# Kernel tuning notes

Hardware: AMD Instinct MI355X
Metric: run time of the kernel (lower is better)

The kernel has to match this reference:

```python
import jax, jax.numpy as jnp
import numpy as np

B, C, H, W = 2, 512, 64, 64
NH = 8
EPS = 1e-5


def setup_inputs() -> dict:
    key = jax.random.key(0)
    ks = jax.random.split(key, 4)
    s_in = 1.0 / np.sqrt(C)
    x = jax.random.normal(ks[0], (B, C, H, W), dtype=jnp.float32)
    qkv_w = jax.random.normal(ks[1], (3 * C, C), dtype=jnp.float32) * s_in
    qkv_b = jnp.zeros((3 * C,), dtype=jnp.float32)
    out_w = jax.random.normal(ks[2], (C, C), dtype=jnp.float32) * s_in
    out_b = jnp.zeros((C,), dtype=jnp.float32)
    ln_g = jnp.ones((C,), dtype=jnp.float32)
    ln_b = jnp.zeros((C,), dtype=jnp.float32)
    return {"x": x, "qkv_w": qkv_w, "qkv_b": qkv_b, "out_w": out_w,
            "out_b": out_b, "ln_g": ln_g, "ln_b": ln_b, "num_heads": NH}


def reference(x, qkv_w, qkv_b, out_w, out_b, ln_g, ln_b, num_heads):
    b, c, h, w = x.shape
    n = h * w
    hd = c // num_heads
    scale = hd ** -0.5

    # flatten spatial: [B, N, C]
    tokens = x.reshape(b, c, n).transpose(0, 2, 1)

    # fused QKV projection
    qkv = tokens @ qkv_w.T + qkv_b            # [B, N, 3C]
    q, k, v = jnp.split(qkv, 3, axis=-1)

    def heads(t):  # [B, N, C] -> [B, H, N, D]
        return t.reshape(b, n, num_heads, hd).transpose(0, 2, 1, 3)

    q, k, v = heads(q), heads(k), heads(v)

    # naive full attention (materializes [B, H, N, N] as in the original)
    scores = jnp.einsum('bhqd,bhkd->bhqk', q, k) * scale
    attn = jax.nn.softmax(scores, axis=-1)
    out = jnp.einsum('bhqk,bhkd->bhqd', attn, v)  # [B, H, N, D]

    out = out.transpose(0, 2, 1, 3).reshape(b, n, c)
    attended = out @ out_w.T + out_b          # [B, N, C]

    # residual + LayerNorm over channels
    res = attended + tokens
    mean = jnp.mean(res, axis=-1, keepdims=True)
    var = jnp.var(res, axis=-1, keepdims=True)
    y = (res - mean) * jax.lax.rsqrt(var + EPS) * ln_g + ln_b

    return y.transpose(0, 2, 1).reshape(b, c, h, w)
```

## Files before the change

### kernel.cpp

```cpp
#include <hip/hip_runtime.h>

#define BATCH 2
#define CH    512
#define NTOK  4096
#define NH    8
#define HD    64
#define MTOT  (BATCH*NTOK)

typedef __attribute__((ext_vector_type(8))) __bf16 bf16x8;
typedef __attribute__((ext_vector_type(4))) float  f32x4;
typedef __attribute__((ext_vector_type(4))) unsigned short u16x4;

static __device__ __forceinline__ f32x4 mfma16(bf16x8 a, bf16x8 b, f32x4 c) {
  return __builtin_amdgcn_mfma_f32_16x16x32_bf16(a, b, c, 0, 0, 0);
}

static __device__ __forceinline__ unsigned short f2bf(float f) {
  unsigned int u = __float_as_uint(f);
  u += 0x7fffu + ((u >> 16) & 1u);
  return (unsigned short)(u >> 16);
}

static __device__ __forceinline__ void gload_lds16(const unsigned short* g, unsigned short* l) {
  __builtin_amdgcn_global_load_lds((const __attribute__((address_space(1))) void*)g,
                                   (__attribute__((address_space(3))) void*)l, 16, 0, 0);
}

#define QSC 0.18033688011112042f

__global__ __launch_bounds__(256) void k_transpose(const float* __restrict__ x,
                                                   unsigned short* __restrict__ tokB) {
  __shared__ float tile[32][33];
  int b  = blockIdx.z;
  int n0 = blockIdx.x * 32;
  int c0 = blockIdx.y * 32;
  int tx = threadIdx.x & 31, ty = threadIdx.x >> 5;
#pragma unroll
  for (int i = 0; i < 4; i++) {
    int c = c0 + ty + 8 * i;
    tile[ty + 8 * i][tx] = x[((size_t)b * CH + c) * NTOK + n0 + tx];
  }
  __syncthreads();
#pragma unroll
  for (int i = 0; i < 4; i++) {
    int n = n0 + ty + 8 * i;
    int c = c0 + tx;
    tokB[((size_t)b * NTOK + n) * CH + c] = f2bf(tile[tx][ty + 8 * i]);
  }
}

__global__ __launch_bounds__(256) void k_castw(const float* __restrict__ w1,
                                               const float* __restrict__ w2,
                                               unsigned short* __restrict__ o1,
                                               unsigned short* __restrict__ o2) {
  int i = blockIdx.x * 256 + threadIdx.x;
  if (i < 3 * CH * CH) o1[i] = f2bf(w1[i]);
  else o2[i - 3 * CH * CH] = f2bf(w2[i - 3 * CH * CH]);
}

#define BK 64

static __device__ __forceinline__ void stage_g(const unsigned short* __restrict__ src,
                                               size_t row0, int k0,
                                               unsigned short* __restrict__ lds,
                                               int wid, int lane) {
  int sub = lane >> 3;
  int ch  = (lane & 7) ^ sub;
#pragma unroll
  for (int i = 0; i < 4; i++) {
    int rbase = 32 * wid + 8 * i;
    gload_lds16(&src[(row0 + rbase + sub) * 512 + k0 + ch * 8], &lds[rbase * BK]);
  }
}

static __device__ __forceinline__ bf16x8 frag_ld(const unsigned short* __restrict__ lds,
                                                 int row, int ks, int lane) {
  int ch = ((ks << 2) + (lane >> 4)) ^ (row & 7);
  return *reinterpret_cast<const bf16x8*>(&lds[row * BK + ch * 8]);
}

__global__ __launch_bounds__(256) void k_gemm_qkv(const unsigned short* __restrict__ A,
                                                  const unsigned short* __restrict__ W,
                                                  const float* __restrict__ bias,
                                                  unsigned short* __restrict__ qb,
                                                  unsigned short* __restrict__ kb,
                                                  unsigned short* __restrict__ vt) {
  __shared__ unsigned short lsA[128 * BK];
  __shared__ unsigned short lsB[128 * BK];
  int bm0 = blockIdx.x * 128;
  int bn0 = blockIdx.y * 128;
  int tid = threadIdx.x, lane = tid & 63, wid = tid >> 6;
  int wm = wid >> 1, wn = wid & 1;

  f32x4 acc[4][4];
  f32x4 zz = {0.f, 0.f, 0.f, 0.f};
#pragma unroll
  for (int i = 0; i < 4; i++)
#pragma unroll
    for (int j = 0; j < 4; j++) acc[i][j] = zz;

  for (int k0 = 0; k0 < 512; k0 += BK) {
    stage_g(A, (size_t)bm0, k0, lsA, wid, lane);
    stage_g(W, (size_t)bn0, k0, lsB, wid, lane);
    __syncthreads();
#pragma unroll
    for (int ks = 0; ks < 2; ks++) {
      bf16x8 af[4], bfr[4];
#pragma unroll
      for (int t = 0; t < 4; t++) {
        af[t]  = frag_ld(lsA, wm * 64 + t * 16 + (lane & 15), ks, lane);
        bfr[t] = frag_ld(lsB, wn * 64 + t * 16 + (lane & 15), ks, lane);
      }
#pragma unroll
      for (int mt = 0; mt < 4; mt++)
#pragma unroll
        for (int nt = 0; nt < 4; nt++) acc[mt][nt] = mfma16(af[mt], bfr[nt], acc[mt][nt]);
    }
    __syncthreads();
  }
#pragma unroll
  for (int nt = 0; nt < 4; nt++) {
    int j = bn0 + wn * 64 + nt * 16 + (lane & 15);
    float bj = bias[j];
    int which = j >> 9;
    int cp = j & 511;
    int h = cp >> 6, d = cp & 63;
    if (which == 2) {
#pragma unroll
      for (int mt = 0; mt < 4; mt++) {
        int m = bm0 + wm * 64 + mt * 16 + 4 * (lane >> 4);
        int b = m >> 12, n = m & 4095;
        u16x4 pk;
#pragma unroll
        for (int r = 0; r < 4; r++) pk[r] = f2bf(acc[mt][nt][r] + bj);
        *reinterpret_cast<u16x4*>(&vt[((size_t)((b * NH + h) * HD + d)) * NTOK + n]) = pk;
      }
    } else {
      unsigned short* dst = (which == 0) ? qb : kb;
      float sc = (which == 0) ? QSC : 1.0f;
#pragma unroll
      for (int mt = 0; mt < 4; mt++) {
#pragma unroll
        for (int r = 0; r < 4; r++) {
          int m = bm0 + wm * 64 + mt * 16 + 4 * (lane >> 4) + r;
          int b = m >> 12, n = m & 4095;
          dst[(((size_t)(b * NH + h) * NTOK + n) << 6) + d] = f2bf((acc[mt][nt][r] + bj) * sc);
        }
      }
    }
  }
}

#define KVB 64
#define NT  (NTOK / KVB)

static __device__ __forceinline__ void stage_kv(const unsigned short* __restrict__ Kp,
                                                const unsigned short* __restrict__ Vp,
                                                unsigned short* __restrict__ lk,
                                                unsigned short* __restrict__ lv,
                                                int kv0, int wid, int lane) {
  int sub = lane >> 3;
  int c7  = lane & 7;
#pragma unroll
  for (int i = 0; i < 2; i++) {
    int rbase = 16 * wid + 8 * i;
    int row = rbase + sub;
    int fk = (sub & 3) | (i << 2);
    gload_lds16(&Kp[((size_t)(kv0 + row) << 6) + ((c7 ^ fk) << 3)], &lk[rbase << 6]);
    gload_lds16(&Vp[(size_t)row * NTOK + kv0 + ((c7 ^ sub) << 3)], &lv[rbase << 6]);
  }
}

static __device__ __forceinline__ void attn_tile(const unsigned short* __restrict__ lk,
                                                 const unsigned short* __restrict__ lv,
                                                 const bf16x8 qf[2][2],
                                                 f32x4* oacc0, f32x4* oacc1,
                                                 f32x4& lacc0, f32x4& lacc1,
                                                 bf16x8 onesf, int g, int lr) {
  f32x4 zz = {0.f, 0.f, 0.f, 0.f};
  int l7 = lr & 7;
  int tbase = 8 * (lr >> 2) + (lr & 3);
  int kc0 = ((g ^ l7) << 3);
  int kc1 = (((4 + g) ^ l7) << 3);
  bf16x8 kf[4][2];
#pragma unroll
  for (int ct = 0; ct < 4; ct++) {
    int t = tbase + 4 * (ct >> 1) + 32 * (ct & 1);
    kf[ct][0] = *reinterpret_cast<const bf16x8*>(&lk[(t << 6) + kc0]);
    kf[ct][1] = *reinterpret_cast<const bf16x8*>(&lk[(t << 6) + kc1]);
  }
  f32x4 s0[4], s1[4];
#pragma unroll
  for (int ct = 0; ct < 4; ct++) {
    s0[ct] = zz; s1[ct] = zz;
#pragma unroll
    for (int ks = 0; ks < 2; ks++) {
      s0[ct] = mfma16(kf[ct][ks], qf[0][ks], s0[ct]);
      s1[ct] = mfma16(kf[ct][ks], qf[1][ks], s1[ct]);
    }
  }
  bf16x8 vf[4][2];
#pragma unroll
  for (int dt = 0; dt < 4; dt++) {
    vf[dt][0] = *reinterpret_cast<const bf16x8*>(&lv[((dt * 16 + lr) << 6) + kc0]);
    vf[dt][1] = *reinterpret_cast<const bf16x8*>(&lv[((dt * 16 + lr) << 6) + kc1]);
  }
#pragma unroll
  for (int ct = 0; ct < 4; ct++) {
#pragma unroll
    for (int r = 0; r < 4; r++) {
      s0[ct][r] = __builtin_exp2f(s0[ct][r]);
      s1[ct][r] = __builtin_exp2f(s1[ct][r]);
    }
  }
  unsigned int w0[4][2], w1[4][2];
#pragma unroll
  for (int ct = 0; ct < 4; ct++) {
    asm("v_cvt_pk_bf16_f32 %0, %1, %2" : "=v"(w0[ct][0]) : "v"(s0[ct][0]), "v"(s0[ct][1]));
    asm("v_cvt_pk_bf16_f32 %0, %1, %2" : "=v"(w0[ct][1]) : "v"(s0[ct][2]), "v"(s0[ct][3]));
    asm("v_cvt_pk_bf16_f32 %0, %1, %2" : "=v"(w1[ct][0]) : "v"(s1[ct][0]), "v"(s1[ct][1]));
    asm("v_cvt_pk_bf16_f32 %0, %1, %2" : "=v"(w1[ct][1]) : "v"(s1[ct][2]), "v"(s1[ct][3]));
  }
  union U { unsigned int w[4]; bf16x8 v; };
  U a0, a1, b0, b1;
  a0.w[0] = w0[0][0]; a0.w[1] = w0[0][1]; a0.w[2] = w0[2][0]; a0.w[3] = w0[2][1];
  a1.w[0] = w0[1][0]; a1.w[1] = w0[1][1]; a1.w[2] = w0[3][0]; a1.w[3] = w0[3][1];
  b0.w[0] = w1[0][0]; b0.w[1] = w1[0][1]; b0.w[2] = w1[2][0]; b0.w[3] = w1[2][1];
  b1.w[0] = w1[1][0]; b1.w[1] = w1[1][1]; b1.w[2] = w1[3][0]; b1.w[3] = w1[3][1];
#pragma unroll
  for (int dt = 0; dt < 4; dt++) {
    oacc0[dt] = mfma16(a0.v, vf[dt][0], oacc0[dt]);
    oacc0[dt] = mfma16(a1.v, vf[dt][1], oacc0[dt]);
    oacc1[dt] = mfma16(b0.v, vf[dt][0], oacc1[dt]);
    oacc1[dt] = mfma16(b1.v, vf[dt][1], oacc1[dt]);
  }
  lacc0 = mfma16(a0.v, onesf, lacc0);
  lacc0 = mfma16(a1.v, onesf, lacc0);
  lacc1 = mfma16(b0.v, onesf, lacc1);
  lacc1 = mfma16(b1.v, onesf, lacc1);
}

__global__ __launch_bounds__(256, 2) void k_attn(const unsigned short* __restrict__ Q,
                                                 const unsigned short* __restrict__ K,
                                                 const unsigned short* __restrict__ Vt,
                                                 unsigned short* __restrict__ O) {
  __shared__ unsigned short lsK[2][KVB * 64];
  __shared__ unsigned short lsV[2][64 * KVB];
  int gid = blockIdx.y * 32 + blockIdx.x;
  int vv  = (gid & 7) * 64 + (gid >> 3);
  int bh  = vv >> 5;
  int tid = threadIdx.x, lane = tid & 63, wid = tid >> 6;
  int g = lane >> 4, lr = lane & 15;
  int qw = (vv & 31) * 128 + wid * 32;
  const unsigned short* Qp = Q + (size_t)bh * NTOK * HD;
  const unsigned short* Kp = K + (size_t)bh * NTOK * HD;
  const unsigned short* Vp = Vt + (size_t)bh * HD * NTOK;
  unsigned short* K0 = &lsK[0][0]; unsigned short* K1 = &lsK[1][0];
  unsigned short* V0 = &lsV[0][0]; unsigned short* V1 = &lsV[1][0];

  union { unsigned short u[8]; bf16x8 v; } ou;
#pragma unroll
  for (int i = 0; i < 8; i++) ou.u[i] = 0x3F80;
  bf16x8 onesf = ou.v;

  bf16x8 qf[2][2];
#pragma unroll
  for (int sq = 0; sq < 2; sq++)
#pragma unroll
    for (int ks = 0; ks < 2; ks++)
      qf[sq][ks] = *reinterpret_cast<const bf16x8*>(
          &Qp[(size_t)(qw + sq * 16 + lr) * HD + ks * 32 + 8 * g]);

  f32x4 zz = {0.f, 0.f, 0.f, 0.f};
  f32x4 oacc0[4] = {zz, zz, zz, zz};
  f32x4 oacc1[4] = {zz, zz, zz, zz};
  f32x4 lacc0 = zz, lacc1 = zz;

  stage_kv(Kp, Vp, K0, V0, 0, wid, lane);
  __syncthreads();

  for (int t = 0; t < NT; t += 2) {
    stage_kv(Kp, Vp, K1, V1, (t + 1) * KVB, wid, lane);
    attn_tile(K0, V0, qf, oacc0, oacc1, lacc0, lacc1, onesf, g, lr);
    __syncthreads();
    if (t + 2 < NT) stage_kv(Kp, Vp, K0, V0, (t + 2) * KVB, wid, lane);
    attn_tile(K1, V1, qf, oacc0, oacc1, lacc0, lacc1, onesf, g, lr);
    __syncthreads();
  }
  int b2 = bh >> 3, h = bh & 7;
#pragma unroll
  for (int sq = 0; sq < 2; sq++) {
    f32x4* oacc = sq ? oacc1 : oacc0;
    f32x4  lacc = sq ? lacc1 : lacc0;
#pragma unroll
    for (int r = 0; r < 4; r++) {
      float inv = 1.0f / lacc[r];
      int n = qw + sq * 16 + 4 * g + r;
#pragma unroll
      for (int dt = 0; dt < 4; dt++) {
        int d = dt * 16 + lr;
        O[((size_t)(b2 * NTOK + n)) * CH + h * HD + d] = f2bf(oacc[dt][r] * inv);
      }
    }
  }
}

__global__ __launch_bounds__(256) void k_gemm_out(const unsigned short* __restrict__ A,
                                                  const unsigned short* __restrict__ W,
                                                  const float* __restrict__ bias,
                                                  const unsigned short* __restrict__ tokB,
                                                  float* __restrict__ res) {
  __shared__ unsigned short lsA[128 * BK];
  __shared__ unsigned short lsB[128 * BK];
  int bm0 = blockIdx.x * 128;
  int bn0 = blockIdx.y * 128;
  int tid = threadIdx.x, lane = tid & 63, wid = tid >> 6;
  int wm = wid >> 1, wn = wid & 1;

  f32x4 acc[4][4];
  f32x4 zz = {0.f, 0.f, 0.f, 0.f};
#pragma unroll
  for (int i = 0; i < 4; i++)
#pragma unroll
    for (int j = 0; j < 4; j++) acc[i][j] = zz;

  for (int k0 = 0; k0 < 512; k0 += BK) {
    stage_g(A, (size_t)bm0, k0, lsA, wid, lane);
    stage_g(W, (size_t)bn0, k0, lsB, wid, lane);
    __syncthreads();
#pragma unroll
    for (int ks = 0; ks < 2; ks++) {
      bf16x8 af[4], bfr[4];
#pragma unroll
      for (int t = 0; t < 4; t++) {
        af[t]  = frag_ld(lsA, wm * 64 + t * 16 + (lane & 15), ks, lane);
        bfr[t] = frag_ld(lsB, wn * 64 + t * 16 + (lane & 15), ks, lane);
      }
#pragma unroll
      for (int mt = 0; mt < 4; mt++)
#pragma unroll
        for (int nt = 0; nt < 4; nt++) acc[mt][nt] = mfma16(af[mt], bfr[nt], acc[mt][nt]);
    }
    __syncthreads();
  }
#pragma unroll
  for (int nt = 0; nt < 4; nt++) {
    int j = bn0 + wn * 64 + nt * 16 + (lane & 15);
    float bj = bias[j];
#pragma unroll
    for (int mt = 0; mt < 4; mt++) {
#pragma unroll
      for (int r = 0; r < 4; r++) {
        int m = bm0 + wm * 64 + mt * 16 + 4 * (lane >> 4) + r;
        size_t idx = (size_t)m * CH + j;
        float tk = __uint_as_float((unsigned int)tokB[idx] << 16);
        res[idx] = acc[mt][nt][r] + bj + tk;
      }
    }
  }
}

__global__ __launch_bounds__(256) void k_ln(const float* __restrict__ res,
                                            const float* __restrict__ g,
                                            const float* __restrict__ bb,
                                            float* __restrict__ y) {
  __shared__ float smean[64], srstd[64];
  int m0 = blockIdx.x * 64;
  int tid = threadIdx.x, lane = tid & 63, wid = tid >> 6;
  for (int t = 0; t < 16; t++) {
    int idx = wid * 16 + t;
    const float* row = res + (size_t)(m0 + idx) * CH;
    float s = 0.f, ss = 0.f;
#pragma unroll
    for (int i = 0; i < 8; i++) {
      float v = row[lane + 64 * i];
      s += v; ss += v * v;
    }
#pragma unroll
    for (int off = 1; off < 64; off <<= 1) {
      s += __shfl_xor(s, off);
      ss += __shfl_xor(ss, off);
    }
    if (lane == 0) {
      float mean = s * (1.0f / CH);
      float var = ss * (1.0f / CH) - mean * mean;
      smean[idx] = mean;
      srstd[idx] = rsqrtf(var + 1e-5f);
    }
  }
  __syncthreads();
  int b = m0 >> 12, n0 = m0 & 4095;
  int tn = tid & 63;
  int cq = tid >> 6;
  float mn = smean[tn], rs = srstd[tn];
  const float* rrow = res + (size_t)(m0 + tn) * CH;
  for (int c = cq; c < CH; c += 4) {
    float v = (rrow[c] - mn) * rs * g[c] + bb[c];
    y[((size_t)b * CH + c) * NTOK + n0 + tn] = v;
  }
}

extern "C" void kernel_launch(void* const* d_in, const int* in_sizes, int n_in,
                              void* d_out, int out_size, void* d_ws, size_t ws_size,
                              hipStream_t stream) {
  const float* x    = (const float*)d_in[0];
  const float* qkvw = (const float*)d_in[1];
  const float* qkvb = (const float*)d_in[2];
  const float* outw = (const float*)d_in[3];
  const float* outb = (const float*)d_in[4];
  const float* lng  = (const float*)d_in[5];
  const float* lnb  = (const float*)d_in[6];
  float* y = (float*)d_out;

  const size_t NC = (size_t)MTOT * CH;
  char* ws = (char*)d_ws;
  size_t off = 0;
  auto nxt = [&](size_t bytes) -> void* {
    void* p = ws + off;
    off += (bytes + 255) & ~(size_t)255;
    return p;
  };
  unsigned short* tokB = (unsigned short*)nxt(NC * 2);
  unsigned short* wqkv = (unsigned short*)nxt((size_t)3 * CH * CH * 2);
  unsigned short* wout = (unsigned short*)nxt((size_t)CH * CH * 2);
  unsigned short* qb   = (unsigned short*)nxt(NC * 2);
  unsigned short* kb   = (unsigned short*)nxt(NC * 2);
  unsigned short* vt   = (unsigned short*)nxt(NC * 2);
  unsigned short* ao   = (unsigned short*)nxt(NC * 2);
  float*          resb = (float*)nxt(NC * 4);
  if (off > ws_size) return;

  k_transpose<<<dim3(NTOK / 32, CH / 32, BATCH), 256, 0, stream>>>(x, tokB);
  k_castw<<<(4 * CH * CH) / 256, 256, 0, stream>>>(qkvw, outw, wqkv, wout);
  k_gemm_qkv<<<dim3(MTOT / 128, (3 * CH) / 128), 256, 0, stream>>>(tokB, wqkv, qkvb, qb, kb, vt);
  k_attn<<<dim3(32, 16), 256, 0, stream>>>(qb, kb, vt, ao);
  k_gemm_out<<<dim3(MTOT / 128, CH / 128), 256, 0, stream>>>(ao, wout, outb, tokB, resb);
  k_ln<<<MTOT / 64, 256, 0, stream>>>(resb, lng, lnb, y);
}
```

Before: 184.5 us.

## Enlarge attention KV tile, halve out-GEMM M tile, store residual in bf16

The attention kernel now stages 128 keys/values per buffer and runs two sub-tiles per barrier, with a new swizzled V layout, so fewer synchronisations and loads are issued per key. The output projection GEMM uses 64-row tiles, which doubles the block count for better occupancy. The residual buffer is stored as bf16 and LayerNorm reads it with vectorized loads, halving that traffic. The cost is lower residual precision before LayerNorm and more LDS per attention block.

Result: faster. 164.0 us (-11.1%).

```diff
diff --git a/kernel.cpp b/kernel.cpp
--- a/kernel.cpp
+++ b/kernel.cpp
@@ -69,6 +69,19 @@
 #pragma unroll
   for (int i = 0; i < 4; i++) {
     int rbase = 32 * wid + 8 * i;
+    gload_lds16(&src[(row0 + rbase + sub) * 512 + k0 + ch * 8], &lds[rbase * BK]);
+  }
+}
+
+static __device__ __forceinline__ void stage_g64(const unsigned short* __restrict__ src,
+                                                 size_t row0, int k0,
+                                                 unsigned short* __restrict__ lds,
+                                                 int wid, int lane) {
+  int sub = lane >> 3;
+  int ch  = (lane & 7) ^ sub;
+#pragma unroll
+  for (int i = 0; i < 2; i++) {
+    int rbase = 16 * wid + 8 * i;
     gload_lds16(&src[(row0 + rbase + sub) * 512 + k0 + ch * 8], &lds[rbase * BK]);
   }
 }
@@ -151,7 +164,7 @@
   }
 }
 
-#define KVB 64
+#define KVB 128
 #define NT  (NTOK / KVB)
 
 static __device__ __forceinline__ void stage_kv(const unsigned short* __restrict__ Kp,
@@ -161,18 +174,22 @@
                                                 int kv0, int wid, int lane) {
   int sub = lane >> 3;
   int c7  = lane & 7;
-#pragma unroll
-  for (int i = 0; i < 2; i++) {
-    int rbase = 16 * wid + 8 * i;
-    int row = rbase + sub;
-    int fk = (sub & 3) | (i << 2);
-    gload_lds16(&Kp[((size_t)(kv0 + row) << 6) + ((c7 ^ fk) << 3)], &lk[rbase << 6]);
-    gload_lds16(&Vp[(size_t)row * NTOK + kv0 + ((c7 ^ sub) << 3)], &lv[rbase << 6]);
+  int sub4 = lane >> 4;
+  int c15  = lane & 15;
+#pragma unroll
+  for (int i = 0; i < 4; i++) {
+    int rbase = 32 * wid + 8 * i;
+    int fk = (sub & 3) | ((i & 1) << 2);
+    gload_lds16(&Kp[((size_t)(kv0 + rbase + sub) << 6) + ((c7 ^ fk) << 3)], &lk[rbase << 6]);
+    int rbv = 16 * wid + 4 * i;
+    int fv = 4 * i + sub4;
+    gload_lds16(&Vp[(size_t)(rbv + sub4) * NTOK + kv0 + ((c15 ^ fv) << 3)], &lv[rbv << 7]);
   }
 }
 
 static __device__ __forceinline__ void attn_tile(const unsigned short* __restrict__ lk,
                                                  const unsigned short* __restrict__ lv,
+                                                 int h,
                                                  const bf16x8 qf[2][2],
                                                  f32x4* oacc0, f32x4* oacc1,
                                                  f32x4& lacc0, f32x4& lacc1,
@@ -202,8 +219,9 @@
   bf16x8 vf[4][2];
 #pragma unroll
   for (int dt = 0; dt < 4; dt++) {
-    vf[dt][0] = *reinterpret_cast<const bf16x8*>(&lv[((dt * 16 + lr) << 6) + kc0]);
-    vf[dt][1] = *reinterpret_cast<const bf16x8*>(&lv[((dt * 16 + lr) << 6) + kc1]);
+    int rowb = (dt * 16 + lr) << 7;
+    vf[dt][0] = *reinterpret_cast<const bf16x8*>(&lv[rowb + ((((h << 3) + g) ^ lr) << 3)]);
+    vf[dt][1] = *reinterpret_cast<const bf16x8*>(&lv[rowb + ((((h << 3) + 4 + g) ^ lr) << 3)]);
   }
 #pragma unroll
   for (int ct = 0; ct < 4; ct++) {
@@ -281,10 +299,12 @@
 
   for (int t = 0; t < NT; t += 2) {
     stage_kv(Kp, Vp, K1, V1, (t + 1) * KVB, wid, lane);
-    attn_tile(K0, V0, qf, oacc0, oacc1, lacc0, lacc1, onesf, g, lr);
+    attn_tile(K0,        V0, 0, qf, oacc0, oacc1, lacc0, lacc1, onesf, g, lr);
+    attn_tile(K0 + 4096, V0, 1, qf, oacc0, oacc1, lacc0, lacc1, onesf, g, lr);
     __syncthreads();
     if (t + 2 < NT) stage_kv(Kp, Vp, K0, V0, (t + 2) * KVB, wid, lane);
-    attn_tile(K1, V1, qf, oacc0, oacc1, lacc0, lacc1, onesf, g, lr);
+    attn_tile(K1,        V1, 0, qf, oacc0, oacc1, lacc0, lacc1, onesf, g, lr);
+    attn_tile(K1 + 4096, V1, 1, qf, oacc0, oacc1, lacc0, lacc1, onesf, g, lr);
     __syncthreads();
   }
   int b2 = bh >> 3, h = bh & 7;
@@ -309,35 +329,36 @@
                                                   const unsigned short* __restrict__ W,
                                                   const float* __restrict__ bias,
                                                   const unsigned short* __restrict__ tokB,
-                                                  float* __restrict__ res) {
-  __shared__ unsigned short lsA[128 * BK];
+                                                  unsigned short* __restrict__ res) {
+  __shared__ unsigned short lsA[64 * BK];
   __shared__ unsigned short lsB[128 * BK];
-  int bm0 = blockIdx.x * 128;
+  int bm0 = blockIdx.x * 64;
   int bn0 = blockIdx.y * 128;
   int tid = threadIdx.x, lane = tid & 63, wid = tid >> 6;
   int wm = wid >> 1, wn = wid & 1;
 
-  f32x4 acc[4][4];
+  f32x4 acc[2][4];
   f32x4 zz = {0.f, 0.f, 0.f, 0.f};
 #pragma unroll
-  for (int i = 0; i < 4; i++)
+  for (int i = 0; i < 2; i++)
 #pragma unroll
     for (int j = 0; j < 4; j++) acc[i][j] = zz;
 
   for (int k0 = 0; k0 < 512; k0 += BK) {
-    stage_g(A, (size_t)bm0, k0, lsA, wid, lane);
+    stage_g64(A, (size_t)bm0, k0, lsA, wid, lane);
     stage_g(W, (size_t)bn0, k0, lsB, wid, lane);
     __syncthreads();
 #pragma unroll
     for (int ks = 0; ks < 2; ks++) {
-      bf16x8 af[4], bfr[4];
-#pragma unroll
-      for (int t = 0; t < 4; t++) {
-        af[t]  = frag_ld(lsA, wm * 64 + t * 16 + (lane & 15), ks, lane);
+      bf16x8 af[2], bfr[4];
+#pragma unroll
+      for (int t = 0; t < 2; t++)
+        af[t] = frag_ld(lsA, wm * 32 + t * 16 + (lane & 15), ks, lane);
+#pragma unroll
+      for (int t = 0; t < 4; t++)
         bfr[t] = frag_ld(lsB, wn * 64 + t * 16 + (lane & 15), ks, lane);
-      }
-#pragma unroll
-      for (int mt = 0; mt < 4; mt++)
+#pragma unroll
+      for (int mt = 0; mt < 2; mt++)
 #pragma unroll
         for (int nt = 0; nt < 4; nt++) acc[mt][nt] = mfma16(af[mt], bfr[nt], acc[mt][nt]);
     }
@@ -348,19 +369,19 @@
     int j = bn0 + wn * 64 + nt * 16 + (lane & 15);
     float bj = bias[j];
 #pragma unroll
-    for (int mt = 0; mt < 4; mt++) {
+    for (int mt = 0; mt < 2; mt++) {
 #pragma unroll
       for (int r = 0; r < 4; r++) {
-        int m = bm0 + wm * 64 + mt * 16 + 4 * (lane >> 4) + r;
+        int m = bm0 + wm * 32 + mt * 16 + 4 * (lane >> 4) + r;
         size_t idx = (size_t)m * CH + j;
         float tk = __uint_as_float((unsigned int)tokB[idx] << 16);
-        res[idx] = acc[mt][nt][r] + bj + tk;
+        res[idx] = f2bf(acc[mt][nt][r] + bj + tk);
       }
     }
   }
 }
 
-__global__ __launch_bounds__(256) void k_ln(const float* __restrict__ res,
+__global__ __launch_bounds__(256) void k_ln(const unsigned short* __restrict__ res,
                                             const float* __restrict__ g,
                                             const float* __restrict__ bb,
                                             float* __restrict__ y) {
@@ -369,12 +390,14 @@
   int tid = threadIdx.x, lane = tid & 63, wid = tid >> 6;
   for (int t = 0; t < 16; t++) {
     int idx = wid * 16 + t;
-    const float* row = res + (size_t)(m0 + idx) * CH;
+    uint4 v = *reinterpret_cast<const uint4*>(&res[(size_t)(m0 + idx) * CH + lane * 8]);
+    unsigned int wv[4] = {v.x, v.y, v.z, v.w};
     float s = 0.f, ss = 0.f;
 #pragma unroll
-    for (int i = 0; i < 8; i++) {
-      float v = row[lane + 64 * i];
-      s += v; ss += v * v;
+    for (int j = 0; j < 4; j++) {
+      float lo = __uint_as_float(wv[j] << 16);
+      float hi = __uint_as_float(wv[j] & 0xFFFF0000u);
+      s += lo + hi; ss += lo * lo + hi * hi;
     }
 #pragma unroll
     for (int off = 1; off < 64; off <<= 1) {
@@ -393,10 +416,26 @@
   int tn = tid & 63;
   int cq = tid >> 6;
   float mn = smean[tn], rs = srstd[tn];
-  const float* rrow = res + (size_t)(m0 + tn) * CH;
-  for (int c = cq; c < CH; c += 4) {
-    float v = (rrow[c] - mn) * rs * g[c] + bb[c];
-    y[((size_t)b * CH + c) * NTOK + n0 + tn] = v;
+  const unsigned short* rrow = res + (size_t)(m0 + tn) * CH;
+  float* yb = y + ((size_t)b * CH) * NTOK + n0 + tn;
+#pragma unroll
+  for (int i = 0; i < 16; i++) {
+    int c = cq * 128 + i * 8;
+    uint4 v = *reinterpret_cast<const uint4*>(&rrow[c]);
+    unsigned int wv[4] = {v.x, v.y, v.z, v.w};
+    float4 ga = *reinterpret_cast<const float4*>(&g[c]);
+    float4 gb = *reinterpret_cast<const float4*>(&g[c + 4]);
+    float4 ba = *reinterpret_cast<const float4*>(&bb[c]);
+    float4 b4 = *reinterpret_cast<const float4*>(&bb[c + 4]);
+    float gg[8] = {ga.x, ga.y, ga.z, ga.w, gb.x, gb.y, gb.z, gb.w};
+    float bv[8] = {ba.x, ba.y, ba.z, ba.w, b4.x, b4.y, b4.z, b4.w};
+#pragma unroll
+    for (int j = 0; j < 4; j++) {
+      float lo = __uint_as_float(wv[j] << 16);
+      float hi = __uint_as_float(wv[j] & 0xFFFF0000u);
+      yb[(size_t)(c + 2 * j) * NTOK]     = (lo - mn) * rs * gg[2 * j]     + bv[2 * j];
+      yb[(size_t)(c + 2 * j + 1) * NTOK] = (hi - mn) * rs * gg[2 * j + 1] + bv[2 * j + 1];
+    }
   }
 }
 
@@ -427,13 +466,13 @@
   unsigned short* kb   = (unsigned short*)nxt(NC * 2);
   unsigned short* vt   = (unsigned short*)nxt(NC * 2);
   unsigned short* ao   = (unsigned short*)nxt(NC * 2);
-  float*          resb = (float*)nxt(NC * 4);
+  unsigned short* resb = (unsigned short*)nxt(NC * 2);
   if (off > ws_size) return;
 
   k_transpose<<<dim3(NTOK / 32, CH / 32, BATCH), 256, 0, stream>>>(x, tokB);
   k_castw<<<(4 * CH * CH) / 256, 256, 0, stream>>>(qkvw, outw, wqkv, wout);
   k_gemm_qkv<<<dim3(MTOT / 128, (3 * CH) / 128), 256, 0, stream>>>(tokB, wqkv, qkvb, qb, kb, vt);
   k_attn<<<dim3(32, 16), 256, 0, stream>>>(qb, kb, vt, ao);
-  k_gemm_out<<<dim3(MTOT / 128, CH / 128), 256, 0, stream>>>(ao, wout, outb, tokB, resb);
+  k_gemm_out<<<dim3(MTOT / 64, CH / 128), 256, 0, stream>>>(ao, wout, outb, tokB, resb);
   k_ln<<<MTOT / 64, 256, 0, stream>>>(resb, lng, lnb, y);
 }
```
